# Kernel tuning notes

Hardware: AMD Instinct MI355X
Metric: run time of the kernel (lower is better)

Reference implementation:

```python
import jax, jax.numpy as jnp
import numpy as np

N_ENTITIES = 100000
EMBED = 64
BATCH = 4096
TEMPERATURE = 0.2


def _infonce(v1, v2, temperature):
    # v1, v2: [B, d]
    B = v1.shape[0]
    sim11 = v1 @ v1.T  # [B,B]
    sim22 = v2 @ v2.T
    sim12 = v1 @ v2.T
    eye = jnp.eye(B, dtype=bool)
    neg_inf = jnp.float32(-jnp.inf)
    sim11 = jnp.where(eye, neg_inf, sim11)
    sim22 = jnp.where(eye, neg_inf, sim22)
    logits1 = jnp.concatenate([sim12, sim11], axis=-1)          # [B,2B]
    logits2 = jnp.concatenate([sim22, sim12.T], axis=-1)        # [B,2B]
    logits = jnp.concatenate([logits1, logits2], axis=0) / temperature  # [2B,2B]
    targets = jnp.arange(2 * B)
    logp = jax.nn.log_softmax(logits, axis=-1)
    return -jnp.mean(jnp.take_along_axis(logp, targets[:, None], axis=-1))


def setup_inputs() -> dict:
    key = jax.random.key(0)
    k1, k2, k3, k4, k5, k6 = jax.random.split(key, 6)
    return {
        "input_u_list": jax.random.randint(k1, (BATCH,), 0, N_ENTITIES),
        "input_i_list": jax.random.randint(k2, (BATCH,), 0, N_ENTITIES),
        "u_sub1_embeddings": jax.random.normal(k3, (N_ENTITIES, EMBED), dtype=jnp.float32),
        "i_sub1_embeddings": jax.random.normal(k4, (N_ENTITIES, EMBED), dtype=jnp.float32),
        "u_sub2_embeddings": jax.random.normal(k5, (N_ENTITIES, EMBED), dtype=jnp.float32),
        "i_sub2_embeddings": jax.random.normal(k6, (N_ENTITIES, EMBED), dtype=jnp.float32),
    }


def reference(input_u_list, input_i_list, u_sub1_embeddings, i_sub1_embeddings,
              u_sub2_embeddings, i_sub2_embeddings):
    # user branch: gather + L2-normalize
    u1 = u_sub1_embeddings[input_u_list]
    u2 = u_sub2_embeddings[input_u_list]
    u1 = u1 / jnp.linalg.norm(u1, axis=1, keepdims=True)
    u2 = u2 / jnp.linalg.norm(u2, axis=1, keepdims=True)
    user_cl_loss = _infonce(u1, u2, TEMPERATURE)
    # item branch: gather only (the original does NOT normalize items)
    i1 = i_sub1_embeddings[input_i_list]
    i2 = i_sub2_embeddings[input_i_list]
    item_cl_loss = _infonce(i1, i2, TEMPERATURE)
    return user_cl_loss + item_cl_loss
```

## Files before the change

kernel.cpp:

```cpp
#include <hip/hip_runtime.h>
#include <hip/hip_bf16.h>
#include <math.h>

#define B_SZ   4096
#define D      64
#define RPB    8192
#define NCHUNK 8
#define TPC    8
#define NPART  16
#define LN2    0.69314718055994531f
#define PRESCALE 2.6857914f

typedef __attribute__((ext_vector_type(8))) short  bf16x8;
typedef __attribute__((ext_vector_type(4))) float  f32x4;

__device__ __forceinline__ float fexp2(float x) { return __builtin_amdgcn_exp2f(x); }


__global__ __launch_bounds__(256) void gather_kernel(
    const int* __restrict__ u_idx, const int* __restrict__ i_idx,
    const float* __restrict__ u1e, const float* __restrict__ i1e,
    const float* __restrict__ u2e, const float* __restrict__ i2e,
    __hip_bfloat16* __restrict__ Xbf, float* __restrict__ dots)
{
    const int tid  = threadIdx.x;
    const int wave = tid >> 6, lane = tid & 63;
    const int g      = blockIdx.x * 4 + wave;
    const int branch = g >> 12;
    const int i      = g & (B_SZ - 1);
    const int idx    = (branch == 0) ? u_idx[i] : i_idx[i];
    const float* s1  = (branch == 0) ? u1e : i1e;
    const float* s2  = (branch == 0) ? u2e : i2e;

    float v1 = s1[(size_t)idx * D + lane];
    float v2 = s2[(size_t)idx * D + lane];
    if (branch == 0) {
        float a = v1 * v1, b = v2 * v2;
        #pragma unroll
        for (int o = 32; o > 0; o >>= 1) {
            a += __shfl_xor(a, o, 64);
            b += __shfl_xor(b, o, 64);
        }
        v1 *= rsqrtf(a);
        v2 *= rsqrtf(b);
    }
    float p = v1 * v2;
    #pragma unroll
    for (int o = 32; o > 0; o >>= 1) p += __shfl_xor(p, o, 64);
    if (lane == 0) dots[g] = p;

    const size_t row1 = (size_t)branch * RPB + i;
    Xbf[row1 * D + lane]          = __float2bfloat16(v1 * PRESCALE);
    Xbf[(row1 + B_SZ) * D + lane] = __float2bfloat16(v2 * PRESCALE);
}

template<int IS_USER>
__global__ __launch_bounds__(256, 3) void gram_lse_kernel(
    const __hip_bfloat16* __restrict__ Xb, float2* __restrict__ P)
{
    __shared__ __align__(16) __hip_bfloat16 Bs[128][72];

    const int tid   = threadIdx.x;
    const int bx    = blockIdx.x;
    const int chunk = blockIdx.y;
    const int r0    = bx * 128;

    const int wave = tid >> 6, lane = tid & 63;
    const int wm = wave >> 1, wn = wave & 1;
    const int quad = lane >> 4, tx = lane & 15;

    #pragma unroll
    for (int p = 0; p < 4; ++p) {
        int e = p * 256 + tid;
        int row = e >> 3, c8 = e & 7;
        *(uint4*)&Bs[row][c8 * 8] =
            *(const uint4*)(Xb + (size_t)(r0 + row) * D + c8 * 8);
    }
    __syncthreads();
    bf16x8 afr[4][2];
    #pragma unroll
    for (int mt = 0; mt < 4; ++mt)
        #pragma unroll
        for (int ks = 0; ks < 2; ++ks)
            afr[mt][ks] = *(const bf16x8*)&Bs[wm * 64 + mt * 16 + tx][ks * 32 + quad * 8];

    float m_run[16], s_run[16];
    #pragma unroll
    for (int r = 0; r < 16; ++r) { m_run[r] = -INFINITY; s_run[r] = 0.f; }

    const int lrq  = wm * 64 + quad * 4;
    const int lcol = wn * 64 + tx;

    for (int t = 0; t < TPC; ++t) {
        const int ct = chunk * TPC + t;
        const int c0 = ct * 128;
        __syncthreads();
        #pragma unroll
        for (int p = 0; p < 4; ++p) {
            int e = p * 256 + tid;
            int row = e >> 3, c8 = e & 7;
            *(uint4*)&Bs[row][c8 * 8] =
                *(const uint4*)(Xb + (size_t)(c0 + row) * D + c8 * 8);
        }
        __syncthreads();

        f32x4 acc[4][4];
        const f32x4 z = {0.f, 0.f, 0.f, 0.f};
        #pragma unroll
        for (int nt = 0; nt < 4; ++nt) {
            const bf16x8 b0 = *(const bf16x8*)&Bs[wn * 64 + nt * 16 + tx][quad * 8];
            #pragma unroll
            for (int mt = 0; mt < 4; ++mt)
                acc[mt][nt] = __builtin_amdgcn_mfma_f32_16x16x32_bf16(afr[mt][0], b0, z, 0, 0, 0);
        }
        #pragma unroll
        for (int nt = 0; nt < 4; ++nt) {
            const bf16x8 b1 = *(const bf16x8*)&Bs[wn * 64 + nt * 16 + tx][32 + quad * 8];
            #pragma unroll
            for (int mt = 0; mt < 4; ++mt)
                acc[mt][nt] = __builtin_amdgcn_mfma_f32_16x16x32_bf16(afr[mt][1], b1, acc[mt][nt], 0, 0, 0);
        }

        const bool diag = (ct == bx);
        #pragma unroll
        for (int mt = 0; mt < 4; ++mt) {
            #pragma unroll
            for (int rr = 0; rr < 4; ++rr) {
                float y0 = acc[mt][0][rr], y1 = acc[mt][1][rr],
                      y2 = acc[mt][2][rr], y3 = acc[mt][3][rr];
                if (diag) {
                    const int dr = lrq + mt * 16 + rr - lcol;
                    if (dr == 0)  y0 = -INFINITY;
                    if (dr == 16) y1 = -INFINITY;
                    if (dr == 32) y2 = -INFINITY;
                    if (dr == 48) y3 = -INFINITY;
                }
                const int r = mt * 4 + rr;
                if (IS_USER) {
                    s_run[r] += fexp2(y0) + fexp2(y1) + fexp2(y2) + fexp2(y3);
                } else {
                    float mx   = fmaxf(fmaxf(y0, y1), fmaxf(y2, y3));
                    float newm = fmaxf(m_run[r], mx);
                    s_run[r] = s_run[r] * fexp2(m_run[r] - newm)
                             + fexp2(y0 - newm) + fexp2(y1 - newm)
                             + fexp2(y2 - newm) + fexp2(y3 - newm);
                    m_run[r] = newm;
                }
            }
        }
    }

    #pragma unroll
    for (int r = 0; r < 16; ++r) {
        float m = IS_USER ? 0.f : m_run[r];
        float s = s_run[r];
        #pragma unroll
        for (int o = 1; o < 16; o <<= 1) {
            if (IS_USER) {
                s += __shfl_xor(s, o, 64);
            } else {
                float om = __shfl_xor(m, o, 64);
                float os = __shfl_xor(s, o, 64);
                float M  = fmaxf(m, om);
                s = s * fexp2(m - M) + os * fexp2(om - M);
                m = M;
            }
        }
        if (tx == 0) {
            const int grow = r0 + wm * 64 + (r >> 2) * 16 + quad * 4 + (r & 3);
            P[(size_t)grow * NPART + chunk * 2 + wn] = make_float2(m, s);
        }
    }
}

__global__ __launch_bounds__(256) void merge_kernel(
    const float2* __restrict__ P, const float* __restrict__ dots,
    float* __restrict__ out)
{
    __shared__ float red[4];
    const int tid  = threadIdx.x;
    const int wave = tid >> 6, lane = tid & 63;
    const int gw   = blockIdx.x * 4 + wave;
    const int row  = gw * 4 + (lane >> 4);
    const int c    = lane & 15;

    float2 p = P[(size_t)row * NPART + c];
    float m = p.x, s = p.y;
    #pragma unroll
    for (int o = 1; o < 16; o <<= 1) {
        float om = __shfl_xor(m, o, 64);
        float os = __shfl_xor(s, o, 64);
        float M  = fmaxf(m, om);
        s = s * fexp2(m - M) + os * fexp2(om - M);
        m = M;
    }

    float v = 0.f;
    if ((lane & 15) == 0)
        v = LN2 * (m + log2f(s)) * (1.0f / (float)RPB);
    if (tid < 8)
        v -= dots[blockIdx.x * 8 + tid] * (5.0f / (float)B_SZ);

    #pragma unroll
    for (int o = 32; o > 0; o >>= 1) v += __shfl_xor(v, o, 64);
    if (lane == 0) red[wave] = v;
    __syncthreads();
    if (tid == 0)
        atomicAdd(out, red[0] + red[1] + red[2] + red[3]);
}

extern "C" void kernel_launch(void* const* d_in, const int* in_sizes, int n_in,
                              void* d_out, int out_size, void* d_ws, size_t ws_size,
                              hipStream_t stream) {
    const int*   u_idx = (const int*)d_in[0];
    const int*   i_idx = (const int*)d_in[1];
    const float* u1e   = (const float*)d_in[2];
    const float* i1e   = (const float*)d_in[3];
    const float* u2e   = (const float*)d_in[4];
    const float* i2e   = (const float*)d_in[5];
    float* out = (float*)d_out;

    __hip_bfloat16* Xbf = (__hip_bfloat16*)d_ws;
    float*  dots = (float*)((char*)d_ws + 2 * RPB * D * 2);
    float2* P    = (float2*)((char*)dots + RPB * sizeof(float));

    hipMemsetAsync(out, 0, sizeof(float), stream);

    gather_kernel<<<dim3(2048), dim3(256), 0, stream>>>(
        u_idx, i_idx, u1e, i1e, u2e, i2e, Xbf, dots);
    gram_lse_kernel<1><<<dim3(64, NCHUNK), dim3(256), 0, stream>>>(Xbf, P);
    gram_lse_kernel<0><<<dim3(64, NCHUNK), dim3(256), 0, stream>>>(
        Xbf + (size_t)RPB * D, P + (size_t)RPB * NPART);
    merge_kernel<<<dim3(1024), dim3(256), 0, stream>>>(P, dots, out);
}
```

Baseline: 176.1 us.

## Fuse gather, gram-LSE and merge into one persistent kernel with grid barriers

Replaces the four launches (memset, gather, two gram/LSE kernels, merge) with one tiny init kernel and a single 512-block kernel. The blocks synchronize through atomic-counter grid barriers between the gather, gram and merge phases, and each block now runs both the user and item gram units in turn. This is meant to remove launch gaps and per-kernel tail effects. In exchange it depends on all 512 blocks being co-resident for the spin barrier to avoid deadlock, and it serializes the two gram units inside each block.

```diff
diff --git a/kernel.cpp b/kernel.cpp
--- a/kernel.cpp
+++ b/kernel.cpp
@@ -10,6 +10,7 @@
 #define NPART  16
 #define LN2    0.69314718055994531f
 #define PRESCALE 2.6857914f
+#define GRID   512
 
 typedef __attribute__((ext_vector_type(8))) short  bf16x8;
 typedef __attribute__((ext_vector_type(4))) float  f32x4;
@@ -17,58 +18,35 @@
 __device__ __forceinline__ float fexp2(float x) { return __builtin_amdgcn_exp2f(x); }
 
 
-__global__ __launch_bounds__(256) void gather_kernel(
-    const int* __restrict__ u_idx, const int* __restrict__ i_idx,
-    const float* __restrict__ u1e, const float* __restrict__ i1e,
-    const float* __restrict__ u2e, const float* __restrict__ i2e,
-    __hip_bfloat16* __restrict__ Xbf, float* __restrict__ dots)
+__device__ __forceinline__ void gsync(unsigned* bar, unsigned target) {
+    __syncthreads();
+    if (threadIdx.x == 0) {
+        __threadfence();
+        __hip_atomic_fetch_add(bar, 1u, __ATOMIC_RELEASE, __HIP_MEMORY_SCOPE_AGENT);
+        while (__hip_atomic_load(bar, __ATOMIC_ACQUIRE, __HIP_MEMORY_SCOPE_AGENT) < target)
+            __builtin_amdgcn_s_sleep(2);
+        __threadfence();
+    }
+    __syncthreads();
+}
+
+__global__ void init_kernel(unsigned* bar, float* out) {
+    *bar = 0u;
+    *out = 0.f;
+}
+
+template<int IS_USER>
+__device__ void gram_unit(const __hip_bfloat16* __restrict__ Xb,
+                          float2* __restrict__ P,
+                          __hip_bfloat16 (&Bs)[128][72],
+                          int bx, int chunk, int tid)
 {
-    const int tid  = threadIdx.x;
-    const int wave = tid >> 6, lane = tid & 63;
-    const int g      = blockIdx.x * 4 + wave;
-    const int branch = g >> 12;
-    const int i      = g & (B_SZ - 1);
-    const int idx    = (branch == 0) ? u_idx[i] : i_idx[i];
-    const float* s1  = (branch == 0) ? u1e : i1e;
-    const float* s2  = (branch == 0) ? u2e : i2e;
-
-    float v1 = s1[(size_t)idx * D + lane];
-    float v2 = s2[(size_t)idx * D + lane];
-    if (branch == 0) {
-        float a = v1 * v1, b = v2 * v2;
-        #pragma unroll
-        for (int o = 32; o > 0; o >>= 1) {
-            a += __shfl_xor(a, o, 64);
-            b += __shfl_xor(b, o, 64);
-        }
-        v1 *= rsqrtf(a);
-        v2 *= rsqrtf(b);
-    }
-    float p = v1 * v2;
-    #pragma unroll
-    for (int o = 32; o > 0; o >>= 1) p += __shfl_xor(p, o, 64);
-    if (lane == 0) dots[g] = p;
-
-    const size_t row1 = (size_t)branch * RPB + i;
-    Xbf[row1 * D + lane]          = __float2bfloat16(v1 * PRESCALE);
-    Xbf[(row1 + B_SZ) * D + lane] = __float2bfloat16(v2 * PRESCALE);
-}
-
-template<int IS_USER>
-__global__ __launch_bounds__(256, 3) void gram_lse_kernel(
-    const __hip_bfloat16* __restrict__ Xb, float2* __restrict__ P)
-{
-    __shared__ __align__(16) __hip_bfloat16 Bs[128][72];
-
-    const int tid   = threadIdx.x;
-    const int bx    = blockIdx.x;
-    const int chunk = blockIdx.y;
-    const int r0    = bx * 128;
-
+    const int r0   = bx * 128;
     const int wave = tid >> 6, lane = tid & 63;
     const int wm = wave >> 1, wn = wave & 1;
     const int quad = lane >> 4, tx = lane & 15;
 
+    __syncthreads();
     #pragma unroll
     for (int p = 0; p < 4; ++p) {
         int e = p * 256 + tid;
@@ -173,33 +151,79 @@
     }
 }
 
-__global__ __launch_bounds__(256) void merge_kernel(
-    const float2* __restrict__ P, const float* __restrict__ dots,
+__global__ __launch_bounds__(256, 2) void fused_kernel(
+    const int* __restrict__ u_idx, const int* __restrict__ i_idx,
+    const float* __restrict__ u1e, const float* __restrict__ i1e,
+    const float* __restrict__ u2e, const float* __restrict__ i2e,
+    __hip_bfloat16* __restrict__ Xbf, float* __restrict__ dots,
+    float2* __restrict__ P, unsigned* __restrict__ bar,
     float* __restrict__ out)
 {
+    __shared__ __align__(16) __hip_bfloat16 Bs[128][72];
     __shared__ float red[4];
+
     const int tid  = threadIdx.x;
     const int wave = tid >> 6, lane = tid & 63;
-    const int gw   = blockIdx.x * 4 + wave;
-    const int row  = gw * 4 + (lane >> 4);
-    const int c    = lane & 15;
-
-    float2 p = P[(size_t)row * NPART + c];
-    float m = p.x, s = p.y;
-    #pragma unroll
-    for (int o = 1; o < 16; o <<= 1) {
-        float om = __shfl_xor(m, o, 64);
-        float os = __shfl_xor(s, o, 64);
-        float M  = fmaxf(m, om);
-        s = s * fexp2(m - M) + os * fexp2(om - M);
-        m = M;
-    }
-
-    float v = 0.f;
-    if ((lane & 15) == 0)
-        v = LN2 * (m + log2f(s)) * (1.0f / (float)RPB);
-    if (tid < 8)
-        v -= dots[blockIdx.x * 8 + tid] * (5.0f / (float)B_SZ);
+
+    #pragma unroll
+    for (int p = 0; p < 4; ++p) {
+        const int g      = (blockIdx.x * 4 + wave) * 4 + p;
+        const int branch = g >> 12;
+        const int i      = g & (B_SZ - 1);
+        const int idx    = (branch == 0) ? u_idx[i] : i_idx[i];
+        const float* s1  = (branch == 0) ? u1e : i1e;
+        const float* s2  = (branch == 0) ? u2e : i2e;
+
+        float v1 = s1[(size_t)idx * D + lane];
+        float v2 = s2[(size_t)idx * D + lane];
+        if (branch == 0) {
+            float a = v1 * v1, b = v2 * v2;
+            #pragma unroll
+            for (int o = 32; o > 0; o >>= 1) {
+                a += __shfl_xor(a, o, 64);
+                b += __shfl_xor(b, o, 64);
+            }
+            v1 *= rsqrtf(a);
+            v2 *= rsqrtf(b);
+        }
+        float pp = v1 * v2;
+        #pragma unroll
+        for (int o = 32; o > 0; o >>= 1) pp += __shfl_xor(pp, o, 64);
+        if (lane == 0) dots[g] = pp;
+
+        const size_t row1 = (size_t)branch * RPB + i;
+        Xbf[row1 * D + lane]          = __float2bfloat16(v1 * PRESCALE);
+        Xbf[(row1 + B_SZ) * D + lane] = __float2bfloat16(v2 * PRESCALE);
+    }
+    gsync(bar, GRID);
+
+    {
+        const int bx = blockIdx.x >> 3, chunk = blockIdx.x & 7;
+        gram_unit<1>(Xbf, P, Bs, bx, chunk, tid);
+        gram_unit<0>(Xbf + (size_t)RPB * D, P + (size_t)RPB * NPART, Bs, bx, chunk, tid);
+    }
+    gsync(bar, 2 * GRID);
+
+    float vsum = 0.f;
+    #pragma unroll
+    for (int pass = 0; pass < 2; ++pass) {
+        const int row = (blockIdx.x * 2 + pass) * 16 + wave * 4 + (lane >> 4);
+        float2 pr = P[(size_t)row * NPART + (lane & 15)];
+        float m = pr.x, s = pr.y;
+        #pragma unroll
+        for (int o = 1; o < 16; o <<= 1) {
+            float om = __shfl_xor(m, o, 64);
+            float os = __shfl_xor(s, o, 64);
+            float M  = fmaxf(m, om);
+            s = s * fexp2(m - M) + os * fexp2(om - M);
+            m = M;
+        }
+        if ((lane & 15) == 0) vsum += LN2 * (m + log2f(s));
+    }
+
+    float v = vsum * (1.0f / (float)RPB);
+    if (tid < 16)
+        v -= dots[blockIdx.x * 16 + tid] * (5.0f / (float)B_SZ);
 
     #pragma unroll
     for (int o = 32; o > 0; o >>= 1) v += __shfl_xor(v, o, 64);
@@ -221,15 +245,11 @@
     float* out = (float*)d_out;
 
     __hip_bfloat16* Xbf = (__hip_bfloat16*)d_ws;
-    float*  dots = (float*)((char*)d_ws + 2 * RPB * D * 2);
-    float2* P    = (float2*)((char*)dots + RPB * sizeof(float));
-
-    hipMemsetAsync(out, 0, sizeof(float), stream);
-
-    gather_kernel<<<dim3(2048), dim3(256), 0, stream>>>(
-        u_idx, i_idx, u1e, i1e, u2e, i2e, Xbf, dots);
-    gram_lse_kernel<1><<<dim3(64, NCHUNK), dim3(256), 0, stream>>>(Xbf, P);
-    gram_lse_kernel<0><<<dim3(64, NCHUNK), dim3(256), 0, stream>>>(
-        Xbf + (size_t)RPB * D, P + (size_t)RPB * NPART);
-    merge_kernel<<<dim3(1024), dim3(256), 0, stream>>>(P, dots, out);
-}
+    float*    dots = (float*)((char*)d_ws + 2 * RPB * D * 2);
+    float2*   P    = (float2*)((char*)dots + RPB * sizeof(float));
+    unsigned* bar  = (unsigned*)((char*)P + (size_t)2 * RPB * NPART * sizeof(float2));
+
+    init_kernel<<<dim3(1), dim3(1), 0, stream>>>(bar, out);
+    fused_kernel<<<dim3(GRID), dim3(256), 0, stream>>>(
+        u_idx, i_idx, u1e, i1e, u2e, i2e, Xbf, dots, P, bar, out);
+}
```

New measurement: 294.8 us. 1.67x slower.
